# Optimization experiments

Hardware: AMD Instinct MI355X
Metric: run time of the kernel (lower is better)

## Reference

```python
import jax, jax.numpy as jnp
import numpy as np

POS_T = 0.7
NEG_T = 0.3
TOTAL = 256      # total_num_samples
MAX_POS = 128    # max_pos_samples
N_ANCH = 262144
N_GT = 256
IMG_H = 1024
IMG_W = 1024


def _make_boxes(key, n, img_h, img_w, min_sz, max_sz):
    # boxes in (y1, x1, y2, x2); some anchors will fall outside the image
    kc, ks = jax.random.split(key)
    cy = jax.random.uniform(kc, (n,)) * img_h
    cx = jax.random.uniform(jax.random.fold_in(kc, 1), (n,)) * img_w
    h = min_sz + jax.random.uniform(ks, (n,)) * (max_sz - min_sz)
    w = min_sz + jax.random.uniform(jax.random.fold_in(ks, 1), (n,)) * (max_sz - min_sz)
    return jnp.stack([cy - h / 2, cx - w / 2, cy + h / 2, cx + w / 2], axis=1).astype(jnp.float32)


def setup_inputs() -> dict:
    key = jax.random.key(0)
    ka, kg = jax.random.split(key)
    anchors = _make_boxes(ka, N_ANCH, IMG_H, IMG_W, 16.0, 512.0)
    gt_bboxes = _make_boxes(kg, N_GT, IMG_H, IMG_W, 32.0, 256.0)
    # keep gt boxes inside the image
    gt_bboxes = jnp.clip(gt_bboxes, 0.0, jnp.array([IMG_H, IMG_W, IMG_H, IMG_W], jnp.float32))
    return {"anchors": anchors, "gt_bboxes": gt_bboxes, "image_h": IMG_H, "image_w": IMG_W}


def _pairwise_iou(boxes_a, boxes_b):
    # boxes_a: [N,4], boxes_b: [M,4] in (y1,x1,y2,x2)
    a = boxes_a[:, None, :]   # [N,1,4]
    b = boxes_b[None, :, :]   # [1,M,4]
    ih = jnp.clip(jnp.minimum(a[..., 2], b[..., 2]) - jnp.maximum(a[..., 0], b[..., 0]), 0.0)
    iw = jnp.clip(jnp.minimum(a[..., 3], b[..., 3]) - jnp.maximum(a[..., 1], b[..., 1]), 0.0)
    inter = ih * iw                                                  # [N,M]
    area_a = (boxes_a[:, 2] - boxes_a[:, 0]) * (boxes_a[:, 3] - boxes_a[:, 1])
    area_b = (boxes_b[:, 2] - boxes_b[:, 0]) * (boxes_b[:, 3] - boxes_b[:, 1])
    union = area_a[:, None] + area_b[None, :] - inter
    return inter / jnp.maximum(union, 1e-8)


def _forward(anchors, gt_bboxes, image_h, image_w):
    n = anchors.shape[0]
    # 1. boundary filter (kept as a mask -> fixed shapes, same semantics:
    #    out-of-image anchors get label -1 and are never sampled)
    inside = ((anchors[:, 0] >= 0) & (anchors[:, 1] >= 0) &
              (anchors[:, 2] <= image_h) & (anchors[:, 3] <= image_w))
    # 2. pairwise IoU   [N, M]
    iou = _pairwise_iou(anchors, gt_bboxes)
    max_ious = jnp.max(iou, axis=1)
    argmax_ious = jnp.argmax(iou, axis=1).astype(jnp.int32)
    # 3. threshold labeling
    labels = jnp.full((n,), -1, jnp.int32)
    labels = jnp.where(max_ious > POS_T, 1, labels)
    labels = jnp.where(max_ious < NEG_T, 0, labels)
    labels = jnp.where(inside, labels, -1)
    pos_mask = labels == 1
    neg_mask = labels == 0
    total_pos = jnp.sum(pos_mask.astype(jnp.int32))
    total_neg = jnp.sum(neg_mask.astype(jnp.int32))
    cur_pos = jnp.minimum(total_pos, MAX_POS)
    cur_neg = jnp.minimum(TOTAL - cur_pos, total_neg)
    # 5. random sampling via random-score top_k (fixed-shape analogue of
    #    tf.random_shuffle + slice)
    kp, kn = jax.random.split(jax.random.key(42))
    pos_scores = jnp.where(pos_mask, jax.random.uniform(kp, (n,)), -1.0)
    neg_scores = jnp.where(neg_mask, jax.random.uniform(kn, (n,)), -1.0)
    _, pos_idx = jax.lax.top_k(pos_scores, MAX_POS)   # original anchor ids
    _, neg_idx = jax.lax.top_k(neg_scores, TOTAL)
    # pack: first cur_pos slots are positives, next cur_neg are negatives,
    # remaining slots padded with -1 (original returns a dynamic-size concat)
    out_idx = jnp.full((TOTAL,), -1, jnp.int32)
    pslot = jnp.where(jnp.arange(MAX_POS) < cur_pos, jnp.arange(MAX_POS), TOTAL)
    out_idx = out_idx.at[pslot].set(pos_idx.astype(jnp.int32), mode='drop')
    nslot = jnp.where(jnp.arange(TOTAL) < cur_neg, cur_pos + jnp.arange(TOTAL), TOTAL)
    out_idx = out_idx.at[nslot].set(neg_idx.astype(jnp.int32), mode='drop')
    safe = jnp.clip(out_idx, 0, n - 1)
    valid = out_idx >= 0
    sel_labels = jnp.where(valid, labels[safe], -1)
    sel_gt = jnp.where(valid, argmax_ious[safe], -1)
    return out_idx, sel_labels, sel_gt, cur_pos


def reference(anchors, gt_bboxes, image_h, image_w):
    return _forward(anchors, gt_bboxes, image_h, image_w)
```

## Files before the change

### kernel.cpp

```cpp
#include <hip/hip_runtime.h>

#pragma clang fp contract(off)

#define N_ANCH   262144
#define N_GT     256
#define MAX_POSK 128
#define TOTALK   256
#define NBINS    2048
#define CAP      2048
#define BORDCAP  2048

struct TF2 { unsigned a, b; };

__host__ __device__ constexpr unsigned rotl32(unsigned v, int d) {
  return (v << d) | (v >> (32 - d));
}

__host__ __device__ constexpr TF2 tf2x32(unsigned k0, unsigned k1,
                                         unsigned x0, unsigned x1) {
  unsigned ks2 = k0 ^ k1 ^ 0x1BD11BDAu;
  x0 += k0; x1 += k1;
  x0 += x1; x1 = rotl32(x1, 13); x1 ^= x0;
  x0 += x1; x1 = rotl32(x1, 15); x1 ^= x0;
  x0 += x1; x1 = rotl32(x1, 26); x1 ^= x0;
  x0 += x1; x1 = rotl32(x1,  6); x1 ^= x0;
  x0 += k1; x1 += ks2 + 1u;
  x0 += x1; x1 = rotl32(x1, 17); x1 ^= x0;
  x0 += x1; x1 = rotl32(x1, 29); x1 ^= x0;
  x0 += x1; x1 = rotl32(x1, 16); x1 ^= x0;
  x0 += x1; x1 = rotl32(x1, 24); x1 ^= x0;
  x0 += ks2; x1 += k0 + 2u;
  x0 += x1; x1 = rotl32(x1, 13); x1 ^= x0;
  x0 += x1; x1 = rotl32(x1, 15); x1 ^= x0;
  x0 += x1; x1 = rotl32(x1, 26); x1 ^= x0;
  x0 += x1; x1 = rotl32(x1,  6); x1 ^= x0;
  x0 += k0; x1 += k1 + 3u;
  x0 += x1; x1 = rotl32(x1, 17); x1 ^= x0;
  x0 += x1; x1 = rotl32(x1, 29); x1 ^= x0;
  x0 += x1; x1 = rotl32(x1, 16); x1 ^= x0;
  x0 += x1; x1 = rotl32(x1, 24); x1 ^= x0;
  x0 += k1; x1 += ks2 + 4u;
  x0 += x1; x1 = rotl32(x1, 13); x1 ^= x0;
  x0 += x1; x1 = rotl32(x1, 15); x1 ^= x0;
  x0 += x1; x1 = rotl32(x1, 26); x1 ^= x0;
  x0 += x1; x1 = rotl32(x1,  6); x1 ^= x0;
  x0 += ks2; x1 += k0 + 5u;
  return TF2{x0, x1};
}

constexpr unsigned KP0 = tf2x32(0u, 42u, 0u, 0u).a;
constexpr unsigned KP1 = tf2x32(0u, 42u, 0u, 0u).b;
constexpr unsigned KN0 = tf2x32(0u, 42u, 0u, 1u).a;
constexpr unsigned KN1 = tf2x32(0u, 42u, 0u, 1u).b;

__device__ inline unsigned score_bits(unsigned k0, unsigned k1, unsigned i) {
  TF2 r = tf2x32(k0, k1, 0u, i);
  return r.a ^ r.b;
}

constexpr double MPOSD = (double)0.7f + 0x1p-25;
constexpr double MNEGD = (double)0.3f - 0x1p-26;
constexpr float CPF = (float)(MPOSD / (1.0 + MPOSD));
constexpr float CNF = (float)(MNEGD / (1.0 + MNEGD));

__device__ unsigned           g_packed[N_ANCH];
__device__ int                g_hist[2][NBINS];
__device__ int                g_cut[2];
__device__ int                g_curpos, g_curneg;
__device__ int                g_cnt[2];
__device__ unsigned long long g_cand[2][CAP];
__device__ int                g_nbord;
__device__ int                g_bord[BORDCAP];

__global__ void k_init() {
  int t = blockIdx.x * blockDim.x + threadIdx.x;
  if (t < 2 * NBINS) (&g_hist[0][0])[t] = 0;
  if (t == 2 * NBINS) { g_cnt[0] = 0; g_cnt[1] = 0; g_nbord = 0; }
}

__device__ inline void finish_anchor(int i, float4 a, float mp, float mn,
                                     float Hf, float Wf) {
  const float A = (a.z - a.x) * (a.w - a.y);
  const float mrp = mp - CPF * A;
  const float mrn = mn - CNF * A;
  const bool inside = (a.x >= 0.0f) && (a.y >= 0.0f) && (a.z <= Hf) && (a.w <= Wf);
  const float band = 0x1.8p-21f * (A + 65536.0f);
  const bool pos = mrp > band;
  const bool nny = mrn > band;
  int lab = pos ? 1 : (nny ? -1 : 0);
  if (!inside) lab = -1;

  unsigned sb = 0u;
  if (lab >= 0) {
    sb = score_bits(lab == 1 ? KP0 : KN0, lab == 1 ? KP1 : KN1, (unsigned)i);
    atomicAdd(&g_hist[lab == 1 ? 0 : 1][sb >> 21], 1);
  }
  g_packed[i] = (sb & ~511u) | (unsigned)(lab + 1);

  if (inside && (fabsf(mrp) <= band || fabsf(mrn) <= band)) {
    int b = atomicAdd(&g_nbord, 1);
    if (b < BORDCAP) g_bord[b] = i;
  }
}

__global__ __launch_bounds__(256) void k_main(const float4* __restrict__ anchors,
                                              const float4* __restrict__ gt,
                                              const int* __restrict__ ph,
                                              const int* __restrict__ pw) {
  __shared__ float4 s_gt[N_GT];
  __shared__ float  s_tp[N_GT];
  __shared__ float  s_tn[N_GT];
  const int tid = threadIdx.x;
  {
    float4 g = gt[tid];
    s_gt[tid] = g;
    float B = (g.z - g.x) * (g.w - g.y);
    s_tp[tid] = CPF * B;
    s_tn[tid] = CNF * B;
  }
  __syncthreads();

  const int i0 = blockIdx.x * 512 + tid;
  const int i1 = i0 + 256;
  const float4 a0 = anchors[i0];
  const float4 a1 = anchors[i1];
  const float Hf = (float)(*ph);
  const float Wf = (float)(*pw);

  float mp0 = -1e30f, mn0 = -1e30f, mp1 = -1e30f, mn1 = -1e30f;
  #pragma unroll 4
  for (int j = 0; j < N_GT; ++j) {
    const float4 b = s_gt[j];
    const float tp = s_tp[j];
    const float tn = s_tn[j];
    float ih0 = fmaxf(fminf(a0.z, b.z) - fmaxf(a0.x, b.x), 0.0f);
    float iw0 = fmaxf(fminf(a0.w, b.w) - fmaxf(a0.y, b.y), 0.0f);
    float in0 = ih0 * iw0;
    mp0 = fmaxf(mp0, in0 - tp);
    mn0 = fmaxf(mn0, in0 - tn);
    float ih1 = fmaxf(fminf(a1.z, b.z) - fmaxf(a1.x, b.x), 0.0f);
    float iw1 = fmaxf(fminf(a1.w, b.w) - fmaxf(a1.y, b.y), 0.0f);
    float in1 = ih1 * iw1;
    mp1 = fmaxf(mp1, in1 - tp);
    mn1 = fmaxf(mn1, in1 - tn);
  }
  finish_anchor(i0, a0, mp0, mn0, Hf, Wf);
  finish_anchor(i1, a1, mp1, mn1, Hf, Wf);
}

__device__ int find_cut(const int* cs, const int* hist, int K) {
  if (K <= 0) return NBINS;
  int suffix = 0, c = 127;
  for (; c >= 0; --c) {
    if (suffix + cs[c] >= K) break;
    suffix += cs[c];
  }
  if (c < 0) return 0;
  for (int b = c * 16 + 15; b >= c * 16; --b) {
    suffix += hist[b];
    if (suffix >= K) return b;
  }
  return c * 16;
}

__global__ __launch_bounds__(128) void k_select(const float4* __restrict__ anchors,
                                                const float4* __restrict__ gt) {
  __shared__ int csp[128], csn[128];
  const int t = threadIdx.x;
  const int wid = t >> 6, lane = t & 63;

  int nb = g_nbord; if (nb > BORDCAP) nb = BORDCAP;
  for (int b = wid; b < nb; b += 2) {
    const int i = g_bord[b];
    const float4 a = anchors[i];
    const float A = (a.z - a.x) * (a.w - a.y);
    bool p = false, nn = false;
    #pragma unroll
    for (int k = 0; k < 4; ++k) {
      const int j = lane + 64 * k;
      float4 bb = gt[j];
      float ih = fmaxf(fminf(a.z, bb.z) - fmaxf(a.x, bb.x), 0.0f);
      float iw = fmaxf(fminf(a.w, bb.w) - fmaxf(a.y, bb.y), 0.0f);
      float inter = ih * iw;
      float Bar = (bb.z - bb.x) * (bb.w - bb.y);
      float uni = (A + Bar) - inter;
      double id = (double)inter, ud = (double)uni;
      p  |= (id >= MPOSD * ud);
      nn |= (id >= MNEGD * ud);
    }
    unsigned long long bp = __ballot(p);
    unsigned long long bn = __ballot(nn);
    if (lane == 0) {
      int newlab = bp ? 1 : (bn ? -1 : 0);
      unsigned old = g_packed[i];
      int oldlab = (int)(old & 3u) - 1;
      if (newlab != oldlab) {
        if (oldlab >= 0) atomicAdd(&g_hist[oldlab == 1 ? 0 : 1][old >> 21], -1);
        unsigned sb = 0u;
        if (newlab >= 0) {
          sb = score_bits(newlab == 1 ? KP0 : KN0, newlab == 1 ? KP1 : KN1, (unsigned)i);
          atomicAdd(&g_hist[newlab == 1 ? 0 : 1][sb >> 21], 1);
        }
        g_packed[i] = (sb & ~511u) | (unsigned)(newlab + 1);
      }
    }
  }
  __syncthreads();

  int sp = 0, sn = 0;
  for (int b2 = t * 16; b2 < t * 16 + 16; ++b2) { sp += g_hist[0][b2]; sn += g_hist[1][b2]; }
  csp[t] = sp; csn[t] = sn;
  __syncthreads();
  if (t == 0) {
    int total_p = 0, total_n = 0;
    for (int c = 0; c < 128; ++c) { total_p += csp[c]; total_n += csn[c]; }
    int cur_pos = total_p < MAX_POSK ? total_p : MAX_POSK;
    int rem = TOTALK - cur_pos;
    int cur_neg = total_n < rem ? total_n : rem;
    g_curpos = cur_pos;
    g_curneg = cur_neg;
    g_cut[0] = find_cut(csp, g_hist[0], cur_pos);
    g_cut[1] = find_cut(csn, g_hist[1], cur_neg);
  }
}

__global__ __launch_bounds__(256) void k_compact() {
  const int i = blockIdx.x * 256 + threadIdx.x;
  const unsigned p = g_packed[i];
  const int lab0 = (int)(p & 3u);
  if (lab0 == 0) return;
  const int s = (lab0 == 2) ? 0 : 1;
  if ((int)(p >> 21) >= g_cut[s]) {
    int q = atomicAdd(&g_cnt[s], 1);
    if (q < CAP)
      g_cand[s][q] = ((unsigned long long)(p >> 9) << 32) | (unsigned)(~i);
  }
}

__global__ __launch_bounds__(1024) void k_final(int* __restrict__ out) {
  __shared__ unsigned long long keys[CAP];
  const int tid = threadIdx.x;
  const int cur_pos = g_curpos;
  const int cur_neg = g_curneg;

  for (int t = tid; t < 3 * TOTALK; t += 1024) out[t] = -1;
  if (tid == 0) out[3 * TOTALK] = cur_pos;

  int Cp = g_cnt[0]; if (Cp > CAP) Cp = CAP;
  for (int t = tid; t < Cp; t += 1024) keys[t] = g_cand[0][t];
  __syncthreads();
  for (int t = tid; t < Cp; t += 1024) {
    unsigned long long me = keys[t];
    int r = 0;
    for (int u = 0; u < Cp; ++u) r += (keys[u] > me);
    if (r < cur_pos) {
      out[r] = (int)(~(unsigned)me);
      out[TOTALK + r] = 1;
    }
  }
  __syncthreads();

  int Cn = g_cnt[1]; if (Cn > CAP) Cn = CAP;
  for (int t = tid; t < Cn; t += 1024) keys[t] = g_cand[1][t];
  __syncthreads();
  for (int t = tid; t < Cn; t += 1024) {
    unsigned long long me = keys[t];
    int r = 0;
    for (int u = 0; u < Cn; ++u) r += (keys[u] > me);
    if (r < cur_neg) {
      out[cur_pos + r] = (int)(~(unsigned)me);
      out[TOTALK + cur_pos + r] = 0;
    }
  }
}

__global__ __launch_bounds__(256) void k_argmax(const float4* __restrict__ anchors,
                                                const float4* __restrict__ gt,
                                                int* __restrict__ out) {
  __shared__ unsigned long long red[256];
  const int slot = blockIdx.x;
  const int j = threadIdx.x;
  const int idx = out[slot];
  if (idx < 0) {
    if (j == 0) out[2 * TOTALK + slot] = -1;
    return;
  }
  const float4 a = anchors[idx];
  const float4 b = gt[j];
  const float A = (a.z - a.x) * (a.w - a.y);
  const float B = (b.z - b.x) * (b.w - b.y);
  float ih = fmaxf(fminf(a.z, b.z) - fmaxf(a.x, b.x), 0.0f);
  float iw = fmaxf(fminf(a.w, b.w) - fmaxf(a.y, b.y), 0.0f);
  float inter = ih * iw;
  float uni = (A + B) - inter;
  float iou = inter / fmaxf(uni, 1e-8f);
  red[j] = ((unsigned long long)__float_as_uint(iou) << 32) | (unsigned)(~j);
  __syncthreads();
  for (int s = 128; s > 0; s >>= 1) {
    if (j < s) { if (red[j + s] > red[j]) red[j] = red[j + s]; }
    __syncthreads();
  }
  if (j == 0) out[2 * TOTALK + slot] = (int)(~(unsigned)red[0]) & 0xFF;
}

extern "C" void kernel_launch(void* const* d_in, const int* in_sizes, int n_in,
                              void* d_out, int out_size, void* d_ws, size_t ws_size,
                              hipStream_t stream) {
  (void)in_sizes; (void)n_in; (void)out_size; (void)d_ws; (void)ws_size;
  const float4* anchors = (const float4*)d_in[0];
  const float4* gt      = (const float4*)d_in[1];
  const int*    ph      = (const int*)d_in[2];
  const int*    pw      = (const int*)d_in[3];
  int*          out     = (int*)d_out;

  k_init   <<<(2 * NBINS + 256) / 256, 256, 0, stream>>>();
  k_main   <<<N_ANCH / 512, 256, 0, stream>>>(anchors, gt, ph, pw);
  k_select <<<1, 128, 0, stream>>>(anchors, gt);
  k_compact<<<N_ANCH / 256, 256, 0, stream>>>();
  k_final  <<<1, 1024, 0, stream>>>(out);
  k_argmax <<<TOTALK, 256, 0, stream>>>(anchors, gt, out);
}
```

Baseline: 110.8 us.

## Fuse select, compact, final sort and argmax into one single-block tail kernel

Merges the border re-check, cut selection, candidate compaction, rank-sort and per-slot argmax into one 1024-thread kernel. Candidates and selected indices now stay in shared memory, and the histogram reset moves to the end of the tail, which removes k_init. This cuts four kernel launches and the global-memory round trips between them. In exchange, the 262144-anchor compaction scan now runs on a single block, and the code relies on the zero-initialised globals being cleared at the end of every call.

```diff
diff --git a/kernel.cpp b/kernel.cpp
--- a/kernel.cpp
+++ b/kernel.cpp
@@ -63,20 +63,10 @@
 constexpr float CPF = (float)(MPOSD / (1.0 + MPOSD));
 constexpr float CNF = (float)(MNEGD / (1.0 + MNEGD));
 
-__device__ unsigned           g_packed[N_ANCH];
-__device__ int                g_hist[2][NBINS];
-__device__ int                g_cut[2];
-__device__ int                g_curpos, g_curneg;
-__device__ int                g_cnt[2];
-__device__ unsigned long long g_cand[2][CAP];
-__device__ int                g_nbord;
-__device__ int                g_bord[BORDCAP];
-
-__global__ void k_init() {
-  int t = blockIdx.x * blockDim.x + threadIdx.x;
-  if (t < 2 * NBINS) (&g_hist[0][0])[t] = 0;
-  if (t == 2 * NBINS) { g_cnt[0] = 0; g_cnt[1] = 0; g_nbord = 0; }
-}
+__device__ unsigned g_packed[N_ANCH];
+__device__ int      g_hist[2][NBINS];
+__device__ int      g_nbord;
+__device__ int      g_bord[BORDCAP];
 
 __device__ inline void finish_anchor(int i, float4 a, float mp, float mn,
                                      float Hf, float Wf) {
@@ -163,14 +153,25 @@
   return c * 16;
 }
 
-__global__ __launch_bounds__(128) void k_select(const float4* __restrict__ anchors,
-                                                const float4* __restrict__ gt) {
-  __shared__ int csp[128], csn[128];
-  const int t = threadIdx.x;
-  const int wid = t >> 6, lane = t & 63;
+__device__ inline unsigned long long shfl_xor_u64(unsigned long long v, int m) {
+  unsigned lo = (unsigned)v, hi = (unsigned)(v >> 32);
+  lo = __shfl_xor(lo, m, 64);
+  hi = __shfl_xor(hi, m, 64);
+  return ((unsigned long long)hi << 32) | lo;
+}
+
+__global__ __launch_bounds__(1024) void k_tail(const float4* __restrict__ anchors,
+                                               const float4* __restrict__ gt,
+                                               int* __restrict__ out) {
+  __shared__ unsigned long long s_keys[2][CAP];
+  __shared__ int s_csp[128], s_csn[128];
+  __shared__ int s_sel[TOTALK];
+  __shared__ int s_cut[2], s_cnt[2], s_cur[2];
+  const int tid  = threadIdx.x;
+  const int wid  = tid >> 6, lane = tid & 63;
 
   int nb = g_nbord; if (nb > BORDCAP) nb = BORDCAP;
-  for (int b = wid; b < nb; b += 2) {
+  for (int b = wid; b < nb; b += 16) {
     const int i = g_bord[b];
     const float4 a = anchors[i];
     const float A = (a.z - a.x) * (a.w - a.y);
@@ -207,100 +208,104 @@
   }
   __syncthreads();
 
-  int sp = 0, sn = 0;
-  for (int b2 = t * 16; b2 < t * 16 + 16; ++b2) { sp += g_hist[0][b2]; sn += g_hist[1][b2]; }
-  csp[t] = sp; csn[t] = sn;
-  __syncthreads();
-  if (t == 0) {
+  if (tid < 128) {
+    int s = 0;
+    for (int b = tid * 16; b < tid * 16 + 16; ++b) s += g_hist[0][b];
+    s_csp[tid] = s;
+  } else if (tid < 256) {
+    int t2 = tid - 128, s = 0;
+    for (int b = t2 * 16; b < t2 * 16 + 16; ++b) s += g_hist[1][b];
+    s_csn[t2] = s;
+  }
+  if (tid < 2) s_cnt[tid] = 0;
+  __syncthreads();
+  if (tid == 0) {
     int total_p = 0, total_n = 0;
-    for (int c = 0; c < 128; ++c) { total_p += csp[c]; total_n += csn[c]; }
+    for (int c = 0; c < 128; ++c) { total_p += s_csp[c]; total_n += s_csn[c]; }
     int cur_pos = total_p < MAX_POSK ? total_p : MAX_POSK;
     int rem = TOTALK - cur_pos;
     int cur_neg = total_n < rem ? total_n : rem;
-    g_curpos = cur_pos;
-    g_curneg = cur_neg;
-    g_cut[0] = find_cut(csp, g_hist[0], cur_pos);
-    g_cut[1] = find_cut(csn, g_hist[1], cur_neg);
-  }
-}
-
-__global__ __launch_bounds__(256) void k_compact() {
-  const int i = blockIdx.x * 256 + threadIdx.x;
-  const unsigned p = g_packed[i];
-  const int lab0 = (int)(p & 3u);
-  if (lab0 == 0) return;
-  const int s = (lab0 == 2) ? 0 : 1;
-  if ((int)(p >> 21) >= g_cut[s]) {
-    int q = atomicAdd(&g_cnt[s], 1);
-    if (q < CAP)
-      g_cand[s][q] = ((unsigned long long)(p >> 9) << 32) | (unsigned)(~i);
-  }
-}
-
-__global__ __launch_bounds__(1024) void k_final(int* __restrict__ out) {
-  __shared__ unsigned long long keys[CAP];
-  const int tid = threadIdx.x;
-  const int cur_pos = g_curpos;
-  const int cur_neg = g_curneg;
-
+    s_cur[0] = cur_pos;
+    s_cur[1] = cur_neg;
+    s_cut[0] = find_cut(s_csp, g_hist[0], cur_pos);
+    s_cut[1] = find_cut(s_csn, g_hist[1], cur_neg);
+  }
+  __syncthreads();
+
+  const int cut0 = s_cut[0], cut1 = s_cut[1];
+  for (int i = tid; i < N_ANCH; i += 1024) {
+    const unsigned p = g_packed[i];
+    const int lab0 = (int)(p & 3u);
+    if (lab0 == 0) continue;
+    const int s = (lab0 == 2) ? 0 : 1;
+    if ((int)(p >> 21) >= (s == 0 ? cut0 : cut1)) {
+      int q = atomicAdd(&s_cnt[s], 1);
+      if (q < CAP)
+        s_keys[s][q] = ((unsigned long long)(p >> 9) << 32) | (unsigned)(~i);
+    }
+  }
+  for (int t = tid; t < TOTALK; t += 1024) s_sel[t] = -1;
   for (int t = tid; t < 3 * TOTALK; t += 1024) out[t] = -1;
+  __syncthreads();
+
+  const int cur_pos = s_cur[0], cur_neg = s_cur[1];
   if (tid == 0) out[3 * TOTALK] = cur_pos;
-
-  int Cp = g_cnt[0]; if (Cp > CAP) Cp = CAP;
-  for (int t = tid; t < Cp; t += 1024) keys[t] = g_cand[0][t];
-  __syncthreads();
+  int Cp = s_cnt[0]; if (Cp > CAP) Cp = CAP;
+  int Cn = s_cnt[1]; if (Cn > CAP) Cn = CAP;
   for (int t = tid; t < Cp; t += 1024) {
-    unsigned long long me = keys[t];
+    unsigned long long me = s_keys[0][t];
     int r = 0;
-    for (int u = 0; u < Cp; ++u) r += (keys[u] > me);
+    for (int u = 0; u < Cp; ++u) r += (s_keys[0][u] > me);
     if (r < cur_pos) {
-      out[r] = (int)(~(unsigned)me);
+      int idx = (int)(~(unsigned)me);
+      s_sel[r] = idx;
+      out[r] = idx;
       out[TOTALK + r] = 1;
     }
   }
-  __syncthreads();
-
-  int Cn = g_cnt[1]; if (Cn > CAP) Cn = CAP;
-  for (int t = tid; t < Cn; t += 1024) keys[t] = g_cand[1][t];
-  __syncthreads();
   for (int t = tid; t < Cn; t += 1024) {
-    unsigned long long me = keys[t];
+    unsigned long long me = s_keys[1][t];
     int r = 0;
-    for (int u = 0; u < Cn; ++u) r += (keys[u] > me);
+    for (int u = 0; u < Cn; ++u) r += (s_keys[1][u] > me);
     if (r < cur_neg) {
-      out[cur_pos + r] = (int)(~(unsigned)me);
+      int idx = (int)(~(unsigned)me);
+      s_sel[cur_pos + r] = idx;
+      out[cur_pos + r] = idx;
       out[TOTALK + cur_pos + r] = 0;
     }
   }
-}
-
-__global__ __launch_bounds__(256) void k_argmax(const float4* __restrict__ anchors,
-                                                const float4* __restrict__ gt,
-                                                int* __restrict__ out) {
-  __shared__ unsigned long long red[256];
-  const int slot = blockIdx.x;
-  const int j = threadIdx.x;
-  const int idx = out[slot];
-  if (idx < 0) {
-    if (j == 0) out[2 * TOTALK + slot] = -1;
-    return;
-  }
-  const float4 a = anchors[idx];
-  const float4 b = gt[j];
-  const float A = (a.z - a.x) * (a.w - a.y);
-  const float B = (b.z - b.x) * (b.w - b.y);
-  float ih = fmaxf(fminf(a.z, b.z) - fmaxf(a.x, b.x), 0.0f);
-  float iw = fmaxf(fminf(a.w, b.w) - fmaxf(a.y, b.y), 0.0f);
-  float inter = ih * iw;
-  float uni = (A + B) - inter;
-  float iou = inter / fmaxf(uni, 1e-8f);
-  red[j] = ((unsigned long long)__float_as_uint(iou) << 32) | (unsigned)(~j);
-  __syncthreads();
-  for (int s = 128; s > 0; s >>= 1) {
-    if (j < s) { if (red[j + s] > red[j]) red[j] = red[j + s]; }
-    __syncthreads();
-  }
-  if (j == 0) out[2 * TOTALK + slot] = (int)(~(unsigned)red[0]) & 0xFF;
+  __syncthreads();
+
+  {
+    const int slot = tid >> 2;
+    const int q    = tid & 3;
+    const int idx  = s_sel[slot];
+    const int safe = idx < 0 ? 0 : idx;
+    const float4 a = anchors[safe];
+    const float A = (a.z - a.x) * (a.w - a.y);
+    unsigned long long key = 0ULL;
+    for (int k = 0; k < 64; ++k) {
+      const int j = q * 64 + k;
+      const float4 b = gt[j];
+      const float B = (b.z - b.x) * (b.w - b.y);
+      float ih = fmaxf(fminf(a.z, b.z) - fmaxf(a.x, b.x), 0.0f);
+      float iw = fmaxf(fminf(a.w, b.w) - fmaxf(a.y, b.y), 0.0f);
+      float inter = ih * iw;
+      float uni = (A + B) - inter;
+      float iou = inter / fmaxf(uni, 1e-8f);
+      unsigned long long kk =
+          ((unsigned long long)__float_as_uint(iou) << 32) | (unsigned)(~j);
+      key = kk > key ? kk : key;
+    }
+    unsigned long long o1 = shfl_xor_u64(key, 1); key = o1 > key ? o1 : key;
+    unsigned long long o2 = shfl_xor_u64(key, 2); key = o2 > key ? o2 : key;
+    if (q == 0 && idx >= 0)
+      out[2 * TOTALK + slot] = (int)(~(unsigned)key) & 0xFF;
+  }
+  __syncthreads();
+
+  for (int t = tid; t < 2 * NBINS; t += 1024) (&g_hist[0][0])[t] = 0;
+  if (tid == 0) g_nbord = 0;
 }
 
 extern "C" void kernel_launch(void* const* d_in, const int* in_sizes, int n_in,
@@ -313,10 +318,6 @@
   const int*    pw      = (const int*)d_in[3];
   int*          out     = (int*)d_out;
 
-  k_init   <<<(2 * NBINS + 256) / 256, 256, 0, stream>>>();
-  k_main   <<<N_ANCH / 512, 256, 0, stream>>>(anchors, gt, ph, pw);
-  k_select <<<1, 128, 0, stream>>>(anchors, gt);
-  k_compact<<<N_ANCH / 256, 256, 0, stream>>>();
-  k_final  <<<1, 1024, 0, stream>>>(out);
-  k_argmax <<<TOTALK, 256, 0, stream>>>(anchors, gt, out);
-}
+  k_main<<<N_ANCH / 512, 256, 0, stream>>>(anchors, gt, ph, pw);
+  k_tail<<<1, 1024, 0, stream>>>(anchors, gt, out);
+}
```

Result: slower. 218.1 us (+96.8%).
